# Kernel optimization log

Measured on AMD Instinct MI355X. Metric: run time of the kernel, lower is better.

The kernel has to match this reference:

```python
import jax, jax.numpy as jnp
import numpy as np

NBITS = 3      # weight LSQ bits
PBITS = 8      # partial-sum LSQ bits
EPS = 1e-5


def round_ste(x):
    # straight-through round: identity gradient
    return x + jax.lax.stop_gradient(jnp.round(x) - x)


def lsq(x, alpha, nbits):
    # learned-step-size quantize/dequantize (symmetric signed)
    qn = -(2 ** (nbits - 1))
    qp = 2 ** (nbits - 1) - 1
    return round_ste(jnp.clip(x / alpha, qn, qp)) * alpha


def split_views(x):
    # x: [B,C,H,W] -> 9 shifted views of the 1-padded input, stacked [9,B,C,H,W]
    B, C, H, W = x.shape
    xp = jnp.pad(x, ((0, 0), (0, 0), (1, 1), (1, 1)))
    views = [xp[:, :, di:di + H, dj:dj + W] for dj in range(3) for di in range(3)]
    return jnp.stack(views, 0)


def split_conv3x3(x, w, wa, pa):
    # 3x3 conv emulated as 9 shifted 1x1 LSQ convs with quantized partial-sum accumulate
    # w: [9,O,C] per-tap 1x1 weights, wa: [9] weight step sizes, pa: [9] psum step sizes
    xs = split_views(x)                                      # [9,B,C,H,W]
    wq = jax.vmap(lambda wk, ak: lsq(wk, ak, NBITS))(w, wa)  # [9,O,C]
    ps = jnp.einsum('kbchw,koc->kbohw', xs, wq)              # 9 partial sums
    psq = lsq(ps, pa[:, None, None, None, None], PBITS)      # PartialSumLSQ each tap
    return psq.sum(0)                                        # accumulate -> [B,O,H,W]


def batchnorm(x, g, b):
    m = x.mean((0, 2, 3), keepdims=True)
    v = x.var((0, 2, 3), keepdims=True)
    return (x - m) / jnp.sqrt(v + EPS) * g[None, :, None, None] + b[None, :, None, None]


def setup_inputs() -> dict:
    key = jax.random.key(0)
    ks = jax.random.split(key, 8)
    B, C, O, H, W = 16, 128, 128, 56, 56
    x = jax.random.normal(ks[0], (B, C, H, W), jnp.float32)
    w1 = jax.random.normal(ks[1], (9, O, C), jnp.float32) * 0.05
    w2 = jax.random.normal(ks[2], (9, O, O), jnp.float32) * 0.05
    qp_w = 2 ** (NBITS - 1) - 1
    wa1 = 2.0 * jnp.mean(jnp.abs(w1), axis=(1, 2)) / np.sqrt(qp_w)
    wa2 = 2.0 * jnp.mean(jnp.abs(w2), axis=(1, 2)) / np.sqrt(qp_w)
    pa1 = jnp.full((9,), 0.05, jnp.float32)
    pa2 = jnp.full((9,), 0.05, jnp.float32)
    g1 = jnp.ones((O,), jnp.float32); b1 = jnp.zeros((O,), jnp.float32)
    g2 = jnp.ones((O,), jnp.float32); b2 = jnp.zeros((O,), jnp.float32)
    return {'x': x, 'w1': w1, 'wa1': wa1, 'pa1': pa1, 'g1': g1, 'b1': b1,
            'w2': w2, 'wa2': wa2, 'pa2': pa2, 'g2': g2, 'b2': b2}


def reference(x, w1, wa1, pa1, g1, b1, w2, wa2, pa2, g2, b2):
    identity = x
    out = split_conv3x3(x, w1, wa1, pa1)
    out = jax.nn.relu(batchnorm(out, g1, b1))
    out = split_conv3x3(out, w2, wa2, pa2)
    out = batchnorm(out, g2, b2)
    return jax.nn.relu(out + identity)
```

## Files before the change

kernel.cpp:

```cpp
#include <hip/hip_runtime.h>
#include <math.h>

typedef _Float16 f16;
typedef _Float16 half8 __attribute__((ext_vector_type(8)));
typedef float floatx16 __attribute__((ext_vector_type(16)));

#define HW_     3136
#define NPC     50176.0f
#define PB      3364
#define PPLANE  53824
#define ASTRIDE ((size_t)2 * PPLANE * 16)

#define SW(c, px) (((px) + ((c) >> 2) + ((c) & 3) * 8) & 63)

__global__ __launch_bounds__(256) void prep_kernel(
        const float* __restrict__ w1, const float* __restrict__ wa1,
        const float* __restrict__ w2, const float* __restrict__ wa2,
        f16* __restrict__ W2a, f16* __restrict__ W2b) {
    const int idx = blockIdx.x * 256 + threadIdx.x;
    const float* w;
    const float* wa;
    f16* o;
    int m;
    if (idx < 18432) { w = w1; wa = wa1; o = W2a; m = idx; }
    else             { w = w2; wa = wa2; o = W2b; m = idx - 18432; }
    const int tap = m >> 11;
    const int r = m & 2047;
    const int k2 = r >> 7;
    const int oc = r & 127;
    const float a = wa[tap];
    const float* src = w + ((size_t)(tap * 128 + oc) * 128 + k2 * 8);
    half8 hv;
#pragma unroll
    for (int j = 0; j < 8; ++j)
        hv[j] = (f16)rintf(fminf(fmaxf(src[j] / a, -4.f), 3.f));
    *(half8*)(o + (size_t)m * 8) = hv;
}

__global__ __launch_bounds__(256) void pad_kernel(char* __restrict__ X2) {
    const int idx = blockIdx.x * 256 + threadIdx.x;
    const int k2 = idx / 3648;
    const int r = idx - k2 * 3648;
    const int b = r / 228;
    const int j = r - b * 228;
    int h, w;
    if (j < 58)        { h = 0;  w = j; }
    else if (j < 116)  { h = 57; w = j - 58; }
    else { const int k = j - 116; h = 1 + (k >> 1); w = (k & 1) * 57; }
    const size_t chunk = (size_t)k2 * PPLANE + (size_t)b * PB + h * 58 + w;
    float4 z = {0.f, 0.f, 0.f, 0.f};
    *(float4*)(X2 + chunk * 16) = z;
}

__global__ __launch_bounds__(256) void pack_kernel(
        const float* __restrict__ x, char* __restrict__ X2,
        float* __restrict__ stats) {
    __shared__ float xs[8192];
    const int t = threadIdx.x;
    const int blk = blockIdx.x;
    if (blk == 0 && t < 512) stats[t] = 0.f;
    const int b = blk / 49;
    const int p0 = (blk - b * 49) * 64;
    const int lane = t & 63, wq = t >> 6;
#pragma unroll
    for (int i = 0; i < 32; ++i) {
        const int c = i * 4 + wq;
        const float v = x[(size_t)(b * 128 + c) * HW_ + p0 + lane];
        xs[c * 64 + SW(c, lane)] = v;
    }
    __syncthreads();
    const int p = p0 + lane;
    const int h = p / 56;
    const int w = p - h * 56;
    const size_t pp = (size_t)b * PB + (h + 1) * 58 + (w + 1);
#pragma unroll
    for (int s = 0; s < 4; ++s) {
        const int cg = s * 4 + wq;
        half8 hv, lv;
#pragma unroll
        for (int j = 0; j < 8; ++j) {
            const int c = cg * 8 + j;
            const float v = xs[c * 64 + SW(c, lane)];
            const f16 hh = (f16)v;
            hv[j] = hh;
            lv[j] = (f16)(v - (float)hh);
        }
        *(half8*)(X2 + ((size_t)cg * PPLANE + pp) * 16) = hv;
        *(half8*)(X2 + ((size_t)(cg + 16) * PPLANE + pp) * 16) = lv;
    }
}

__global__ __launch_bounds__(256, 2) void conv_kernel(
        const char* __restrict__ X2, const char* __restrict__ W2,
        const float* __restrict__ wav, const float* __restrict__ pav,
        float* __restrict__ cbuf, float* __restrict__ stats) {
    __shared__ float red[512];
    const int t = threadIdx.x;
    const int lane = t & 63;
    const int wv = t >> 6;
    const int wm = wv & 1, wn = wv >> 1;
    const int tile = (blockIdx.x & 7) * 49 + (blockIdx.x >> 3);
    const int kh = lane >> 5;
    const int ln = lane & 31;

    int ppad[2];
#pragma unroll
    for (int mt = 0; mt < 2; ++mt) {
        const int gp = tile * 128 + wm * 64 + mt * 32 + ln;
        const int b = gp / HW_;
        const int p = gp - b * HW_;
        const int h = p / 56;
        const int w = p - h * 56;
        ppad[mt] = b * PB + (h + 1) * 58 + (w + 1);
    }
    int bb2[2];
#pragma unroll
    for (int nt = 0; nt < 2; ++nt)
        bb2[nt] = (kh * 128 + wn * 64 + nt * 32 + ln) * 16;

    floatx16 facc[2][2];
#pragma unroll
    for (int mt = 0; mt < 2; ++mt)
#pragma unroll
        for (int nt = 0; nt < 2; ++nt)
#pragma unroll
            for (int r = 0; r < 16; ++r) facc[mt][nt][r] = 0.f;

    for (int tap = 0; tap < 9; ++tap) {
        const int di = tap - (tap / 3) * 3 - 1;
        const int dj = tap / 3 - 1;
        const float pak = pav[tap];
        const float s1 = wav[tap] / pak;
        const int doff = di * 58 + dj;

        const char* wt = W2 + tap * 32768;
        half8 bfr[2][8];
#pragma unroll
        for (int nt = 0; nt < 2; ++nt)
#pragma unroll
            for (int kf = 0; kf < 8; ++kf)
                bfr[nt][kf] = *(const half8*)(wt + bb2[nt] + kf * 4096);

        size_t aoff[2];
#pragma unroll
        for (int mt = 0; mt < 2; ++mt)
            aoff[mt] = ((size_t)(ppad[mt] + doff) + (size_t)kh * PPLANE) * 16;

        half8 afr[2][4];
#pragma unroll
        for (int s0 = 0; s0 < 4; ++s0)
#pragma unroll
            for (int mt = 0; mt < 2; ++mt)
                afr[mt][s0] = *(const half8*)(X2 + aoff[mt] + (size_t)s0 * ASTRIDE);

        floatx16 acc[2][2];
#pragma unroll
        for (int mt = 0; mt < 2; ++mt)
#pragma unroll
            for (int nt = 0; nt < 2; ++nt)
#pragma unroll
                for (int r = 0; r < 16; ++r) acc[mt][nt][r] = 0.f;

#pragma unroll
        for (int s = 0; s < 16; ++s) {
#pragma unroll
            for (int nt = 0; nt < 2; ++nt)
#pragma unroll
                for (int mt = 0; mt < 2; ++mt)
                    acc[mt][nt] = __builtin_amdgcn_mfma_f32_32x32x16_f16(
                        afr[mt][s & 3], bfr[nt][s & 7], acc[mt][nt], 0, 0, 0);
            if (s < 12) {
#pragma unroll
                for (int mt = 0; mt < 2; ++mt)
                    afr[mt][s & 3] =
                        *(const half8*)(X2 + aoff[mt] + (size_t)(s + 4) * ASTRIDE);
            }
        }

#pragma unroll
        for (int mt = 0; mt < 2; ++mt)
#pragma unroll
            for (int nt = 0; nt < 2; ++nt)
#pragma unroll
                for (int r = 0; r < 16; ++r) {
                    const float q =
                        rintf(fminf(fmaxf(acc[mt][nt][r] * s1, -128.f), 127.f));
                    facc[mt][nt][r] = fmaf(q, pak, facc[mt][nt][r]);
                }
    }

    const int gpb = tile * 128 + wm * 64;
    const int ocb = wn * 64 + ln;
#pragma unroll
    for (int mt = 0; mt < 2; ++mt)
#pragma unroll
        for (int r = 0; r < 16; ++r) {
            const int row = (r & 3) + 8 * (r >> 2) + 4 * kh;
            const int gp = gpb + mt * 32 + row;
            float* rp = cbuf + (size_t)gp * 128 + ocb;
            rp[0]  = facc[mt][0][r];
            rp[32] = facc[mt][1][r];
        }

    float sv[2], qv[2];
#pragma unroll
    for (int nt = 0; nt < 2; ++nt) {
        float s = 0.f, q = 0.f;
#pragma unroll
        for (int mt = 0; mt < 2; ++mt)
#pragma unroll
            for (int r = 0; r < 16; ++r) {
                const float v = facc[mt][nt][r];
                s += v;
                q = fmaf(v, v, q);
            }
        s += __shfl_xor(s, 32, 64);
        q += __shfl_xor(q, 32, 64);
        sv[nt] = s; qv[nt] = q;
    }
    if (lane < 32) {
#pragma unroll
        for (int nt = 0; nt < 2; ++nt) {
            const int oc = wn * 64 + nt * 32 + lane;
            red[oc * 2 + wm] = sv[nt];
            red[256 + oc * 2 + wm] = qv[nt];
        }
    }
    __syncthreads();
    if (t < 128) {
        atomicAdd(&stats[t],       red[2 * t] + red[2 * t + 1]);
        atomicAdd(&stats[128 + t], red[256 + 2 * t] + red[256 + 2 * t + 1]);
    }
}

__global__ __launch_bounds__(256) void bn_split_kernel(
        const float* __restrict__ cbuf, const float* __restrict__ stats,
        const float* __restrict__ g, const float* __restrict__ bb,
        char* __restrict__ X2) {
    __shared__ float xs[8192];
    __shared__ float scs[128], shs[128];
    const int t = threadIdx.x;
    if (t < 128) {
        const float m = stats[t] * (1.f / NPC);
        const float var = stats[128 + t] * (1.f / NPC) - m * m;
        const float inv = 1.f / sqrtf(var + 1e-5f);
        const float sc = g[t] * inv;
        scs[t] = sc;
        shs[t] = bb[t] - m * sc;
    }
    __syncthreads();
    const int blk = blockIdx.x;
#pragma unroll
    for (int i = 0; i < 8; ++i) {
        const int idx = i * 256 + t;
        const int px = idx >> 5;
        const int q = idx & 31;
        const float4 v = *(const float4*)&cbuf[(size_t)(blk * 64 + px) * 128 + q * 4];
        const float vv[4] = {v.x, v.y, v.z, v.w};
#pragma unroll
        for (int j = 0; j < 4; ++j) {
            const int c = q * 4 + j;
            const float y = fmaxf(fmaf(vv[j], scs[c], shs[c]), 0.f);
            xs[c * 64 + SW(c, px)] = y;
        }
    }
    __syncthreads();
    const int b = blk / 49;
    const int p0 = (blk - b * 49) * 64;
    const int lane = t & 63, wq = t >> 6;
    const int p = p0 + lane;
    const int h = p / 56;
    const int w = p - h * 56;
    const size_t pp = (size_t)b * PB + (h + 1) * 58 + (w + 1);
#pragma unroll
    for (int s = 0; s < 4; ++s) {
        const int cg = s * 4 + wq;
        half8 hv, lv;
#pragma unroll
        for (int j = 0; j < 8; ++j) {
            const int c = cg * 8 + j;
            const float v = xs[c * 64 + SW(c, lane)];
            const f16 hh = (f16)v;
            hv[j] = hh;
            lv[j] = (f16)(v - (float)hh);
        }
        *(half8*)(X2 + ((size_t)cg * PPLANE + pp) * 16) = hv;
        *(half8*)(X2 + ((size_t)(cg + 16) * PPLANE + pp) * 16) = lv;
    }
}

__global__ __launch_bounds__(256) void final_kernel(
        const float* __restrict__ cbuf, const float* __restrict__ stats,
        const float* __restrict__ g, const float* __restrict__ bb,
        const float* __restrict__ resid, float* __restrict__ out) {
    __shared__ float xs[8192];
    __shared__ float scs[128], shs[128];
    const int t = threadIdx.x;
    if (t < 128) {
        const float m = stats[t] * (1.f / NPC);
        const float var = stats[128 + t] * (1.f / NPC) - m * m;
        const float inv = 1.f / sqrtf(var + 1e-5f);
        const float sc = g[t] * inv;
        scs[t] = sc;
        shs[t] = bb[t] - m * sc;
    }
    __syncthreads();
    const int blk = blockIdx.x;
#pragma unroll
    for (int i = 0; i < 8; ++i) {
        const int idx = i * 256 + t;
        const int px = idx >> 5;
        const int q = idx & 31;
        const float4 v = *(const float4*)&cbuf[(size_t)(blk * 64 + px) * 128 + q * 4];
        const float vv[4] = {v.x, v.y, v.z, v.w};
#pragma unroll
        for (int j = 0; j < 4; ++j) {
            const int c = q * 4 + j;
            xs[c * 64 + SW(c, px)] = fmaf(vv[j], scs[c], shs[c]);
        }
    }
    __syncthreads();
    const int b = blk / 49;
    const int p0 = (blk - b * 49) * 64;
    const int lane = t & 63, wq = t >> 6;
#pragma unroll
    for (int i = 0; i < 32; ++i) {
        const int c = i * 4 + wq;
        const float v = xs[c * 64 + SW(c, lane)];
        const size_t gi = (size_t)(b * 128 + c) * HW_ + p0 + lane;
        out[gi] = fmaxf(v + resid[gi], 0.f);
    }
}

extern "C" void kernel_launch(void* const* d_in, const int* in_sizes, int n_in,
                              void* d_out, int out_size, void* d_ws, size_t ws_size,
                              hipStream_t stream) {
    const float* x   = (const float*)d_in[0];
    const float* w1  = (const float*)d_in[1];
    const float* wa1 = (const float*)d_in[2];
    const float* pa1 = (const float*)d_in[3];
    const float* g1  = (const float*)d_in[4];
    const float* b1  = (const float*)d_in[5];
    const float* w2  = (const float*)d_in[6];
    const float* wa2 = (const float*)d_in[7];
    const float* pa2 = (const float*)d_in[8];
    const float* g2  = (const float*)d_in[9];
    const float* b2  = (const float*)d_in[10];
    float* out = (float*)d_out;

    char* ws = (char*)d_ws;
    char*  X2    = ws;
    float* cbuf  = (float*)(ws + 27557888);
    f16*   W2a   = (f16*)(ws + 53248000);
    f16*   W2b   = (f16*)(ws + 53542912);
    float* stats = (float*)(ws + 53837824);
    float* stats1 = stats;
    float* stats2 = stats + 256;

    hipLaunchKernelGGL(prep_kernel, dim3(144), dim3(256), 0, stream,
                       w1, wa1, w2, wa2, W2a, W2b);
    hipLaunchKernelGGL(pad_kernel, dim3(456), dim3(256), 0, stream, X2);
    hipLaunchKernelGGL(pack_kernel, dim3(784), dim3(256), 0, stream,
                       x, X2, stats);
    hipLaunchKernelGGL(conv_kernel, dim3(392), dim3(256), 0, stream,
                       X2, (const char*)W2a, wa1, pa1, cbuf, stats1);
    hipLaunchKernelGGL(bn_split_kernel, dim3(784), dim3(256), 0, stream,
                       cbuf, stats1, g1, b1, X2);
    hipLaunchKernelGGL(conv_kernel, dim3(392), dim3(256), 0, stream,
                       X2, (const char*)W2b, wa2, pa2, cbuf, stats2);
    hipLaunchKernelGGL(final_kernel, dim3(784), dim3(256), 0, stream,
                       cbuf, stats2, g2, b2, x, out);
}
```

Baseline: 233.2 us.

## Prefetch next tap's fragments in conv loop and drop LDS transposes in pack kernels

The conv kernel now loads the next tap's weight fragments and the first A fragments inside the current tap's MFMA loop, and fully unrolls the tap loop. This is meant to hide global-load latency between taps. The pack and bn_split kernels no longer transpose through shared memory; each thread reads float4 vectors directly and writes the half8 hi/lo chunks. The cost is higher register pressure in the conv kernel, which could reduce occupancy, and a different global access pattern in the pack kernels.

```diff
diff --git a/kernel.cpp b/kernel.cpp
--- a/kernel.cpp
+++ b/kernel.cpp
@@ -55,38 +55,37 @@
 __global__ __launch_bounds__(256) void pack_kernel(
         const float* __restrict__ x, char* __restrict__ X2,
         float* __restrict__ stats) {
-    __shared__ float xs[8192];
     const int t = threadIdx.x;
-    const int blk = blockIdx.x;
-    if (blk == 0 && t < 512) stats[t] = 0.f;
-    const int b = blk / 49;
-    const int p0 = (blk - b * 49) * 64;
-    const int lane = t & 63, wq = t >> 6;
-#pragma unroll
-    for (int i = 0; i < 32; ++i) {
-        const int c = i * 4 + wq;
-        const float v = x[(size_t)(b * 128 + c) * HW_ + p0 + lane];
-        xs[c * 64 + SW(c, lane)] = v;
-    }
-    __syncthreads();
-    const int p = p0 + lane;
-    const int h = p / 56;
-    const int w = p - h * 56;
-    const size_t pp = (size_t)b * PB + (h + 1) * 58 + (w + 1);
-#pragma unroll
-    for (int s = 0; s < 4; ++s) {
-        const int cg = s * 4 + wq;
+    if (blockIdx.x == 0 && t < 512) stats[t] = 0.f;
+    const int idx = blockIdx.x * 256 + t;
+    const int cg = idx / 12544;
+    const int pg = idx - cg * 12544;
+    const int p  = pg * 4;
+    const int b  = p / HW_;
+    const int pi = p - b * HW_;
+    float v[8][4];
+    const float* xb = x + (size_t)(b * 128 + cg * 8) * HW_ + pi;
+#pragma unroll
+    for (int j = 0; j < 8; ++j) {
+        const float4 t4 = *(const float4*)(xb + (size_t)j * HW_);
+        v[j][0] = t4.x; v[j][1] = t4.y; v[j][2] = t4.z; v[j][3] = t4.w;
+    }
+#pragma unroll
+    for (int i = 0; i < 4; ++i) {
+        const int pp = pi + i;
+        const int h = pp / 56;
+        const int w = pp - h * 56;
+        const size_t chunk = (size_t)b * PB + (h + 1) * 58 + (w + 1);
         half8 hv, lv;
 #pragma unroll
         for (int j = 0; j < 8; ++j) {
-            const int c = cg * 8 + j;
-            const float v = xs[c * 64 + SW(c, lane)];
-            const f16 hh = (f16)v;
+            const float val = v[j][i];
+            const f16 hh = (f16)val;
             hv[j] = hh;
-            lv[j] = (f16)(v - (float)hh);
-        }
-        *(half8*)(X2 + ((size_t)cg * PPLANE + pp) * 16) = hv;
-        *(half8*)(X2 + ((size_t)(cg + 16) * PPLANE + pp) * 16) = lv;
+            lv[j] = (f16)(val - (float)hh);
+        }
+        *(half8*)(X2 + ((size_t)cg * PPLANE + chunk) * 16) = hv;
+        *(half8*)(X2 + ((size_t)(cg + 16) * PPLANE + chunk) * 16) = lv;
     }
 }
 
@@ -126,32 +125,38 @@
 #pragma unroll
             for (int r = 0; r < 16; ++r) facc[mt][nt][r] = 0.f;
 
+    size_t aoff[2], aoffn[2];
+#pragma unroll
+    for (int mt = 0; mt < 2; ++mt)
+        aoff[mt] = ((size_t)(ppad[mt] + (-1) * 58 + (-1)) + (size_t)kh * PPLANE) * 16;
+
+    half8 afr[2][4];
+#pragma unroll
+    for (int s0 = 0; s0 < 4; ++s0)
+#pragma unroll
+        for (int mt = 0; mt < 2; ++mt)
+            afr[mt][s0] = *(const half8*)(X2 + aoff[mt] + (size_t)s0 * ASTRIDE);
+
+    half8 bfr[2][8];
+#pragma unroll
+    for (int nt = 0; nt < 2; ++nt)
+#pragma unroll
+        for (int kf = 0; kf < 8; ++kf)
+            bfr[nt][kf] = *(const half8*)(W2 + bb2[nt] + kf * 4096);
+
+#pragma unroll
     for (int tap = 0; tap < 9; ++tap) {
-        const int di = tap - (tap / 3) * 3 - 1;
-        const int dj = tap / 3 - 1;
         const float pak = pav[tap];
         const float s1 = wav[tap] / pak;
-        const int doff = di * 58 + dj;
-
-        const char* wt = W2 + tap * 32768;
-        half8 bfr[2][8];
-#pragma unroll
-        for (int nt = 0; nt < 2; ++nt)
-#pragma unroll
-            for (int kf = 0; kf < 8; ++kf)
-                bfr[nt][kf] = *(const half8*)(wt + bb2[nt] + kf * 4096);
-
-        size_t aoff[2];
-#pragma unroll
-        for (int mt = 0; mt < 2; ++mt)
-            aoff[mt] = ((size_t)(ppad[mt] + doff) + (size_t)kh * PPLANE) * 16;
-
-        half8 afr[2][4];
-#pragma unroll
-        for (int s0 = 0; s0 < 4; ++s0)
+        if (tap < 8) {
+            const int din = (tap + 1) % 3 - 1;
+            const int djn = (tap + 1) / 3 - 1;
+            const int dn = din * 58 + djn;
 #pragma unroll
             for (int mt = 0; mt < 2; ++mt)
-                afr[mt][s0] = *(const half8*)(X2 + aoff[mt] + (size_t)s0 * ASTRIDE);
+                aoffn[mt] = ((size_t)(ppad[mt] + dn) + (size_t)kh * PPLANE) * 16;
+        }
+        const char* wtn = W2 + (tap + 1) * 32768;
 
         floatx16 acc[2][2];
 #pragma unroll
@@ -174,6 +179,17 @@
                 for (int mt = 0; mt < 2; ++mt)
                     afr[mt][s & 3] =
                         *(const half8*)(X2 + aoff[mt] + (size_t)(s + 4) * ASTRIDE);
+            } else if (tap < 8) {
+#pragma unroll
+                for (int mt = 0; mt < 2; ++mt)
+                    afr[mt][s & 3] =
+                        *(const half8*)(X2 + aoffn[mt] + (size_t)(s - 12) * ASTRIDE);
+            }
+            if (tap < 8 && s >= 8) {
+                const int kf = s - 8;
+#pragma unroll
+                for (int nt = 0; nt < 2; ++nt)
+                    bfr[nt][kf] = *(const half8*)(wtn + bb2[nt] + kf * 4096);
             }
         }
 
@@ -187,6 +203,8 @@
                         rintf(fminf(fmaxf(acc[mt][nt][r] * s1, -128.f), 127.f));
                     facc[mt][nt][r] = fmaf(q, pak, facc[mt][nt][r]);
                 }
+        aoff[0] = aoffn[0];
+        aoff[1] = aoffn[1];
     }
 
     const int gpb = tile * 128 + wm * 64;
@@ -237,7 +255,6 @@
         const float* __restrict__ cbuf, const float* __restrict__ stats,
         const float* __restrict__ g, const float* __restrict__ bb,
         char* __restrict__ X2) {
-    __shared__ float xs[8192];
     __shared__ float scs[128], shs[128];
     const int t = threadIdx.x;
     if (t < 128) {
@@ -249,43 +266,42 @@
         shs[t] = bb[t] - m * sc;
     }
     __syncthreads();
-    const int blk = blockIdx.x;
-#pragma unroll
-    for (int i = 0; i < 8; ++i) {
-        const int idx = i * 256 + t;
-        const int px = idx >> 5;
-        const int q = idx & 31;
-        const float4 v = *(const float4*)&cbuf[(size_t)(blk * 64 + px) * 128 + q * 4];
-        const float vv[4] = {v.x, v.y, v.z, v.w};
-#pragma unroll
-        for (int j = 0; j < 4; ++j) {
-            const int c = q * 4 + j;
-            const float y = fmaxf(fmaf(vv[j], scs[c], shs[c]), 0.f);
-            xs[c * 64 + SW(c, px)] = y;
-        }
-    }
-    __syncthreads();
-    const int b = blk / 49;
-    const int p0 = (blk - b * 49) * 64;
-    const int lane = t & 63, wq = t >> 6;
-    const int p = p0 + lane;
-    const int h = p / 56;
-    const int w = p - h * 56;
-    const size_t pp = (size_t)b * PB + (h + 1) * 58 + (w + 1);
-#pragma unroll
-    for (int s = 0; s < 4; ++s) {
-        const int cg = s * 4 + wq;
+    const int idx = blockIdx.x * 256 + t;
+    const int pg = idx >> 4;
+    const int cg = idx & 15;
+    const int p = pg * 4;
+    const int b = p / HW_;
+    const int pi = p - b * HW_;
+    const float4 s0 = *(const float4*)&scs[cg * 8];
+    const float4 s1 = *(const float4*)&scs[cg * 8 + 4];
+    const float4 h0 = *(const float4*)&shs[cg * 8];
+    const float4 h1 = *(const float4*)&shs[cg * 8 + 4];
+#pragma unroll
+    for (int i = 0; i < 4; ++i) {
+        const float4 va = *(const float4*)&cbuf[(size_t)(p + i) * 128 + cg * 8];
+        const float4 vb = *(const float4*)&cbuf[(size_t)(p + i) * 128 + cg * 8 + 4];
+        float y[8];
+        y[0] = fmaxf(fmaf(va.x, s0.x, h0.x), 0.f);
+        y[1] = fmaxf(fmaf(va.y, s0.y, h0.y), 0.f);
+        y[2] = fmaxf(fmaf(va.z, s0.z, h0.z), 0.f);
+        y[3] = fmaxf(fmaf(va.w, s0.w, h0.w), 0.f);
+        y[4] = fmaxf(fmaf(vb.x, s1.x, h1.x), 0.f);
+        y[5] = fmaxf(fmaf(vb.y, s1.y, h1.y), 0.f);
+        y[6] = fmaxf(fmaf(vb.z, s1.z, h1.z), 0.f);
+        y[7] = fmaxf(fmaf(vb.w, s1.w, h1.w), 0.f);
         half8 hv, lv;
 #pragma unroll
         for (int j = 0; j < 8; ++j) {
-            const int c = cg * 8 + j;
-            const float v = xs[c * 64 + SW(c, lane)];
-            const f16 hh = (f16)v;
+            const f16 hh = (f16)y[j];
             hv[j] = hh;
-            lv[j] = (f16)(v - (float)hh);
-        }
-        *(half8*)(X2 + ((size_t)cg * PPLANE + pp) * 16) = hv;
-        *(half8*)(X2 + ((size_t)(cg + 16) * PPLANE + pp) * 16) = lv;
+            lv[j] = (f16)(y[j] - (float)hh);
+        }
+        const int pp = pi + i;
+        const int h = pp / 56;
+        const int w = pp - h * 56;
+        const size_t chunk = (size_t)b * PB + (h + 1) * 58 + (w + 1);
+        *(half8*)(X2 + ((size_t)cg * PPLANE + chunk) * 16) = hv;
+        *(half8*)(X2 + ((size_t)(cg + 16) * PPLANE + chunk) * 16) = lv;
     }
 }
 
```

New measurement: 267.7 us. +14.8%, slower.

## Stage conv weights in LDS via async copy and prefetch next tap's activations

Applied to the files above, without the earlier changes.

Conv weights for each tap are now brought into a double-buffered shared-memory area with asynchronous global-to-LDS copies, issued one tap ahead. Activation fragments are deepened to 8 in flight, and the loads for the next tap's first fragments overlap the tail of the current tap. The goal is to hide global memory latency between taps and cut register pressure from holding all B fragments. In exchange it adds a barrier per tap and 64KB of LDS, which may limit occupancy to two blocks per CU. The pack kernel also drops its LDS transpose and reads input directly with strided loads.

```diff
diff --git a/kernel.cpp b/kernel.cpp
--- a/kernel.cpp
+++ b/kernel.cpp
@@ -4,14 +4,21 @@
 typedef _Float16 f16;
 typedef _Float16 half8 __attribute__((ext_vector_type(8)));
 typedef float floatx16 __attribute__((ext_vector_type(16)));
+typedef unsigned int u32;
 
 #define HW_     3136
 #define NPC     50176.0f
 #define PB      3364
 #define PPLANE  53824
-#define ASTRIDE ((size_t)2 * PPLANE * 16)
+#define ASTRIDE (2 * PPLANE * 16)
 
 #define SW(c, px) (((px) + ((c) >> 2) + ((c) & 3) * 8) & 63)
+
+typedef __attribute__((address_space(3))) u32 lds_u32;
+typedef __attribute__((address_space(1))) u32 glb_u32;
+__device__ __forceinline__ void async_copy16(const void* g, void* l) {
+    __builtin_amdgcn_global_load_lds((const glb_u32*)g, (lds_u32*)l, 16, 0, 0);
+}
 
 __global__ __launch_bounds__(256) void prep_kernel(
         const float* __restrict__ w1, const float* __restrict__ wa1,
@@ -55,32 +62,25 @@
 __global__ __launch_bounds__(256) void pack_kernel(
         const float* __restrict__ x, char* __restrict__ X2,
         float* __restrict__ stats) {
-    __shared__ float xs[8192];
     const int t = threadIdx.x;
     const int blk = blockIdx.x;
     if (blk == 0 && t < 512) stats[t] = 0.f;
     const int b = blk / 49;
     const int p0 = (blk - b * 49) * 64;
-    const int lane = t & 63, wq = t >> 6;
-#pragma unroll
-    for (int i = 0; i < 32; ++i) {
-        const int c = i * 4 + wq;
-        const float v = x[(size_t)(b * 128 + c) * HW_ + p0 + lane];
-        xs[c * 64 + SW(c, lane)] = v;
-    }
-    __syncthreads();
-    const int p = p0 + lane;
+    const int px = t & 63;
+    const int cq = t >> 6;
+    const int p = p0 + px;
     const int h = p / 56;
     const int w = p - h * 56;
     const size_t pp = (size_t)b * PB + (h + 1) * 58 + (w + 1);
+    const float* xb = x + (size_t)b * 128 * HW_ + p;
 #pragma unroll
     for (int s = 0; s < 4; ++s) {
-        const int cg = s * 4 + wq;
+        const int cg = s * 4 + cq;
         half8 hv, lv;
 #pragma unroll
         for (int j = 0; j < 8; ++j) {
-            const int c = cg * 8 + j;
-            const float v = xs[c * 64 + SW(c, lane)];
+            const float v = xb[(size_t)(cg * 8 + j) * HW_];
             const f16 hh = (f16)v;
             hv[j] = hh;
             lv[j] = (f16)(v - (float)hh);
@@ -94,6 +94,7 @@
         const char* __restrict__ X2, const char* __restrict__ W2,
         const float* __restrict__ wav, const float* __restrict__ pav,
         float* __restrict__ cbuf, float* __restrict__ stats) {
+    __shared__ f16 Bls[2][16384];
     __shared__ float red[512];
     const int t = threadIdx.x;
     const int lane = t & 63;
@@ -113,10 +114,11 @@
         const int w = p - h * 56;
         ppad[mt] = b * PB + (h + 1) * 58 + (w + 1);
     }
-    int bb2[2];
+    int bdsoff[2];
 #pragma unroll
     for (int nt = 0; nt < 2; ++nt)
-        bb2[nt] = (kh * 128 + wn * 64 + nt * 32 + ln) * 16;
+        bdsoff[nt] = (kh * 128 + wn * 64 + nt * 32 + ln) * 16;
+    const int sbase = wv * 8;
 
     floatx16 facc[2][2];
 #pragma unroll
@@ -126,32 +128,46 @@
 #pragma unroll
             for (int r = 0; r < 16; ++r) facc[mt][nt][r] = 0.f;
 
+#pragma unroll
+    for (int i = 0; i < 8; ++i)
+        async_copy16(W2 + (((sbase + i) * 64 + lane) << 4),
+                     (void*)&Bls[0][(sbase + i) * 512]);
+    int aoff[2], aoffn[2];
+#pragma unroll
+    for (int mt = 0; mt < 2; ++mt) {
+        aoff[mt] = ((ppad[mt] - 59) + kh * PPLANE) << 4;
+        aoffn[mt] = aoff[mt];
+    }
+    half8 afr[2][8];
+#pragma unroll
+    for (int s0 = 0; s0 < 8; ++s0)
+#pragma unroll
+        for (int mt = 0; mt < 2; ++mt)
+            afr[mt][s0] = *(const half8*)(X2 + aoff[mt] + s0 * ASTRIDE);
+    __syncthreads();
+
     for (int tap = 0; tap < 9; ++tap) {
-        const int di = tap - (tap / 3) * 3 - 1;
-        const int dj = tap / 3 - 1;
         const float pak = pav[tap];
         const float s1 = wav[tap] / pak;
-        const int doff = di * 58 + dj;
-
-        const char* wt = W2 + tap * 32768;
-        half8 bfr[2][8];
+        const char* bcur = (const char*)&Bls[tap & 1][0];
+        if (tap < 8) {
+            const char* wt = W2 + (tap + 1) * 32768;
+            f16* bnxt = &Bls[(tap + 1) & 1][0];
+#pragma unroll
+            for (int i = 0; i < 8; ++i)
+                async_copy16(wt + (((sbase + i) * 64 + lane) << 4),
+                             (void*)&bnxt[(sbase + i) * 512]);
+            const int dn = ((tap + 1) % 3 - 1) * 58 + ((tap + 1) / 3 - 1);
+#pragma unroll
+            for (int mt = 0; mt < 2; ++mt)
+                aoffn[mt] = ((ppad[mt] + dn) + kh * PPLANE) << 4;
+        }
+        half8 bds[2][2];
 #pragma unroll
         for (int nt = 0; nt < 2; ++nt)
 #pragma unroll
-            for (int kf = 0; kf < 8; ++kf)
-                bfr[nt][kf] = *(const half8*)(wt + bb2[nt] + kf * 4096);
-
-        size_t aoff[2];
-#pragma unroll
-        for (int mt = 0; mt < 2; ++mt)
-            aoff[mt] = ((size_t)(ppad[mt] + doff) + (size_t)kh * PPLANE) * 16;
-
-        half8 afr[2][4];
-#pragma unroll
-        for (int s0 = 0; s0 < 4; ++s0)
-#pragma unroll
-            for (int mt = 0; mt < 2; ++mt)
-                afr[mt][s0] = *(const half8*)(X2 + aoff[mt] + (size_t)s0 * ASTRIDE);
+            for (int sl = 0; sl < 2; ++sl)
+                bds[nt][sl] = *(const half8*)(bcur + sl * 4096 + bdsoff[nt]);
 
         floatx16 acc[2][2];
 #pragma unroll
@@ -168,12 +184,24 @@
 #pragma unroll
                 for (int mt = 0; mt < 2; ++mt)
                     acc[mt][nt] = __builtin_amdgcn_mfma_f32_32x32x16_f16(
-                        afr[mt][s & 3], bfr[nt][s & 7], acc[mt][nt], 0, 0, 0);
-            if (s < 12) {
+                        afr[mt][s & 7], bds[nt][s & 1], acc[mt][nt], 0, 0, 0);
+            if (s <= 13) {
+                const int kf2 = (s + 2) & 7;
+#pragma unroll
+                for (int nt = 0; nt < 2; ++nt)
+                    bds[nt][s & 1] =
+                        *(const half8*)(bcur + kf2 * 4096 + bdsoff[nt]);
+            }
+            if (s < 8) {
 #pragma unroll
                 for (int mt = 0; mt < 2; ++mt)
-                    afr[mt][s & 3] =
-                        *(const half8*)(X2 + aoff[mt] + (size_t)(s + 4) * ASTRIDE);
+                    afr[mt][s & 7] =
+                        *(const half8*)(X2 + aoff[mt] + (s + 8) * ASTRIDE);
+            } else if (tap < 8) {
+#pragma unroll
+                for (int mt = 0; mt < 2; ++mt)
+                    afr[mt][s & 7] =
+                        *(const half8*)(X2 + aoffn[mt] + (s - 8) * ASTRIDE);
             }
         }
 
@@ -187,6 +215,9 @@
                         rintf(fminf(fmaxf(acc[mt][nt][r] * s1, -128.f), 127.f));
                     facc[mt][nt][r] = fmaf(q, pak, facc[mt][nt][r]);
                 }
+        aoff[0] = aoffn[0];
+        aoff[1] = aoffn[1];
+        __syncthreads();
     }
 
     const int gpb = tile * 128 + wm * 64;
@@ -260,26 +291,26 @@
 #pragma unroll
         for (int j = 0; j < 4; ++j) {
             const int c = q * 4 + j;
-            const float y = fmaxf(fmaf(vv[j], scs[c], shs[c]), 0.f);
-            xs[c * 64 + SW(c, px)] = y;
+            xs[c * 64 + SW(c, px)] = fmaxf(fmaf(vv[j], scs[c], shs[c]), 0.f);
         }
     }
     __syncthreads();
     const int b = blk / 49;
     const int p0 = (blk - b * 49) * 64;
-    const int lane = t & 63, wq = t >> 6;
-    const int p = p0 + lane;
+    const int px = t & 63;
+    const int cq = t >> 6;
+    const int p = p0 + px;
     const int h = p / 56;
     const int w = p - h * 56;
     const size_t pp = (size_t)b * PB + (h + 1) * 58 + (w + 1);
 #pragma unroll
     for (int s = 0; s < 4; ++s) {
-        const int cg = s * 4 + wq;
+        const int cg = s * 4 + cq;
         half8 hv, lv;
 #pragma unroll
         for (int j = 0; j < 8; ++j) {
             const int c = cg * 8 + j;
-            const float v = xs[c * 64 + SW(c, lane)];
+            const float v = xs[c * 64 + SW(c, px)];
             const f16 hh = (f16)v;
             hv[j] = hh;
             lv[j] = (f16)(v - (float)hh);
```

Result: faster. 212.6 us (-8.9%).
